# Performance work log

Measured on AMD Instinct MI355X. Metric: run time of the kernel, lower is better.

## Reference

```python
import jax, jax.numpy as jnp
import numpy as np

RNN_DIM = 256
HN_DIM = 2 * RNN_DIM            # bidirectional
EMB = 300                       # WORD_VEC_DIM
VD = 256                        # visual_dim
NHEAD = 2
DH = VD // NHEAD
N, SEQ, VH, VW = 16, 20, 32, 32
EPS = 1e-5


def layernorm(x, g, b):
    m = jnp.mean(x, axis=-1, keepdims=True)
    v = jnp.var(x, axis=-1, keepdims=True)
    return (x - m) * jax.lax.rsqrt(v + EPS) * g + b


def generate_spatial(n, vh, vw):
    # standard 8-dim spatial coordinate features (text_objseg style)
    w = np.arange(vw, dtype=np.float32)
    h = np.arange(vh, dtype=np.float32)
    xmin = w / vw * 2 - 1; xmax = (w + 1) / vw * 2 - 1
    ymin = h / vh * 2 - 1; ymax = (h + 1) / vh * 2 - 1
    f = np.zeros((vh, vw, 8), np.float32)
    f[..., 0] = xmin[None, :]; f[..., 1] = ymin[:, None]
    f[..., 2] = xmax[None, :]; f[..., 3] = ymax[:, None]
    f[..., 4] = (xmin + xmax)[None, :] / 2; f[..., 5] = (ymin + ymax)[:, None] / 2
    f[..., 6] = 1.0 / vw; f[..., 7] = 1.0 / vh
    return np.broadcast_to(f, (n, vh, vw, 8))  # NHWC


def setup_inputs():
    key = jax.random.key(0)
    ks = jax.random.split(key, 12)
    s = 0.02
    return {
        "hs": jax.random.normal(ks[0], (N, SEQ, HN_DIM), jnp.float32),
        "hn": jax.random.normal(ks[1], (N, HN_DIM), jnp.float32),
        "feature": jax.random.normal(ks[2], (N, VD, VH, VW), jnp.float32),
        "embedding": jax.random.normal(ks[3], (N, SEQ, EMB), jnp.float32),
        "words": jax.random.randint(ks[4], (N, SEQ), 0, 100, jnp.int32),
        "qconv_w": jax.random.normal(ks[5], (VD, EMB), jnp.float32) * s,
        "qconv_b": jnp.zeros((VD,), jnp.float32),
        "mconv_w": jax.random.normal(ks[6], (VD, VD + 8 + HN_DIM, 3, 3), jnp.float32) * s,
        "mnorm_g": jnp.ones((VD,), jnp.float32), "mnorm_b": jnp.zeros((VD,), jnp.float32),
        "in_proj_w": jax.random.normal(ks[7], (3 * VD, VD), jnp.float32) * s,
        "in_proj_b": jnp.zeros((3 * VD,), jnp.float32),
        "out_proj_w": jax.random.normal(ks[8], (VD, VD), jnp.float32) * s,
        "out_proj_b": jnp.zeros((VD,), jnp.float32),
        "norm_g": jnp.ones((VD,), jnp.float32), "norm_b": jnp.zeros((VD,), jnp.float32),
        "lin1_w": jax.random.normal(ks[9], (VD, VD), jnp.float32) * s,
        "lin1_b": jnp.zeros((VD,), jnp.float32),
        "lin2_w": jax.random.normal(ks[10], (VD, VD), jnp.float32) * s,
        "lin2_b": jnp.zeros((VD,), jnp.float32),
        "normf_g": jnp.ones((VD,), jnp.float32), "normf_b": jnp.zeros((VD,), jnp.float32),
    }


def _forward(hs, hn, feature, embedding, words,
             qconv_w, qconv_b, mconv_w, mnorm_g, mnorm_b,
             in_proj_w, in_proj_b, out_proj_w, out_proj_b,
             norm_g, norm_b, lin1_w, lin1_b, lin2_w, lin2_b, normf_g, normf_b):
    Nn, C, vh, vw = feature.shape
    P = vh * vw
    spatial = jnp.asarray(generate_spatial(Nn, vh, vw)).transpose(0, 3, 1, 2)  # (N,8,vh,vw)
    hn_rep = jnp.broadcast_to(hn[:, :, None, None], (Nn, hn.shape[1], vh, vw))
    Wq, Wk, Wv = jnp.split(in_proj_w, 3, axis=0)
    bq, bk, bv = jnp.split(in_proj_b, 3, axis=0)
    scale = 1.0 / np.sqrt(DH)

    def step(feat, xs):
        emb_n, active = xs  # emb_n: (N,EMB), active: bool scalar (words[0,n] != 0)
        q = jax.nn.relu(emb_n @ qconv_w.T + qconv_b)            # (N,VD)
        Q = jnp.broadcast_to(q[:, None, :], (Nn, P, VD))
        t = jnp.concatenate([feat, spatial, hn_rep], axis=1)    # (N,VD+8+HN,vh,vw)
        t = jax.lax.conv_general_dilated(t, mconv_w, (1, 1), "SAME",
                                         dimension_numbers=("NCHW", "OIHW", "NCHW"))
        t = jax.nn.relu(t).transpose(0, 2, 3, 1).reshape(Nn, P, VD)
        t = layernorm(t, mnorm_g, mnorm_b)                      # V = K = t
        # torch nn.MultiheadAttention default batch_first=False:
        # axis0 (=N) is the sequence axis, axis1 (=P) is the batch axis.
        qh = (Q @ Wq.T + bq).reshape(Nn, P, NHEAD, DH)
        kh = (t @ Wk.T + bk).reshape(Nn, P, NHEAD, DH)
        vv = (t @ Wv.T + bv).reshape(Nn, P, NHEAD, DH)
        attn = jax.nn.softmax(jnp.einsum("lphd,mphd->phlm", qh, kh) * scale, axis=-1)
        o = jnp.einsum("phlm,mphd->lphd", attn, vv).reshape(Nn, P, VD)
        fea = layernorm(t + (o @ out_proj_w.T + out_proj_b), norm_g, norm_b)
        f2 = jax.nn.relu(fea @ lin1_w.T + lin1_b) @ lin2_w.T + lin2_b
        fea = layernorm(fea + f2, normf_g, normf_b)
        new_feat = fea.transpose(0, 2, 1).reshape(Nn, VD, vh, vw)
        return jnp.where(active, new_feat, feat), None

    xs = (embedding.transpose(1, 0, 2), words[0, :] != 0)
    feat, _ = jax.lax.scan(step, feature, xs)
    return feat


def reference(hs, hn, feature, embedding, words,
              qconv_w, qconv_b, mconv_w, mnorm_g, mnorm_b,
              in_proj_w, in_proj_b, out_proj_w, out_proj_b,
              norm_g, norm_b, lin1_w, lin1_b, lin2_w, lin2_b, normf_g, normf_b):
    return _forward(hs, hn, feature, embedding, words,
                    qconv_w, qconv_b, mconv_w, mnorm_g, mnorm_b,
                    in_proj_w, in_proj_b, out_proj_w, out_proj_b,
                    norm_g, norm_b, lin1_w, lin1_b, lin2_w, lin2_b, normf_g, normf_b)
```

## Files before the change

### kernel.cpp

```cpp
#include <hip/hip_runtime.h>
#include <hip/hip_bf16.h>
#include <cstddef>

typedef __hip_bfloat16 bf16;
typedef short short8 __attribute__((ext_vector_type(8)));
typedef short short4v __attribute__((ext_vector_type(4)));
typedef float float4v __attribute__((ext_vector_type(4)));
#define DEV static __device__ __forceinline__

constexpr int NB = 16;
constexpr int SEQL = 20;
constexpr int CD = 256;
constexpr int PP = 1024;
constexpr int HND = 512;
constexpr int EMBD = 300;
constexpr int CIN = 776;

constexpr size_t SZB = (size_t)NB * PP * CD / 2;
constexpr size_t OF_FEATB = 0;
constexpr size_t OF_TB   = 1*SZB;
constexpr size_t OF_KHB  = 2*SZB;
constexpr size_t OF_VVB  = 3*SZB;
constexpr size_t OF_QH   = 7*SZB;
constexpr size_t OF_HNW  = OF_QH  + (size_t)SEQL*NB*CD;
constexpr size_t OF_SCV  = OF_HNW + (size_t)9*NB*CD;
constexpr size_t OF_WRG  = OF_SCV + (size_t)PP*CD;
constexpr size_t OF_AW   = OF_WRG + (size_t)9*CD*HND;
constexpr size_t OF_PK   = OF_AW  + (size_t)294912;
constexpr size_t OF_FLAG = OF_PK  + (size_t)163840;

DEV float bf2f(bf16 v) { return __bfloat162float(v); }
DEV bf16 f2bf(float v) { return __float2bfloat16(v); }
DEV float sh2f(short v) { bf16 t; *(short*)&t = v; return __bfloat162float(t); }
DEV short f2sh(float v) { bf16 t = f2bf(v); return *(const short*)&t; }

DEV float LD(const void* p, size_t i, int bf) {
  return bf ? __bfloat162float(((const bf16*)p)[i]) : ((const float*)p)[i];
}
DEV int get_bf(const float* ws) { return ((const int*)ws)[OF_FLAG]; }

__global__ void k_detect(const void* g, float* ws) {
  if (threadIdx.x == 0 && blockIdx.x == 0) {
    unsigned w = *(const unsigned*)g;
    ((int*)ws)[OF_FLAG] = ((w & 0xFFFFu) != 0u) ? 1 : 0;
  }
}

DEV void ln_reduce512(const float* tile, float* red, int tid) {
  const int x = tid & 31, seg = tid >> 5;
  float s = 0.f, sq = 0.f;
#pragma unroll
  for (int i = 0; i < 16; ++i) {
    float v = tile[(seg*16 + i)*33 + x];
    s += v; sq += v*v;
  }
  red[seg*32 + x] = s;
  red[512 + seg*32 + x] = sq;
  __syncthreads();
  if (tid < 32) {
    float ts = 0.f, tq = 0.f;
#pragma unroll
    for (int g = 0; g < 16; ++g) { ts += red[g*32 + tid]; tq += red[512 + g*32 + tid]; }
    float m = ts * (1.f/CD);
    float var = tq * (1.f/CD) - m*m;
    red[1024 + tid] = m;
    red[1056 + tid] = 1.f / sqrtf(var + 1e-5f);
  }
  __syncthreads();
}

DEV void mfma_core512(const short* __restrict__ As, const short* __restrict__ PKg,
                      int w, int lane, float4v acc[2][2]) {
  const int xb = lane & 15, quad = lane >> 4;
  const short* base = PKg + lane*8;
  short8 b0[8], b1[8];
#pragma unroll
  for (int ch = 0; ch < 8; ++ch) {
    b0[ch] = *(const short8*)&base[(size_t)((w*2+0)*8 + ch)*512];
    b1[ch] = *(const short8*)&base[(size_t)((w*2+1)*8 + ch)*512];
  }
#pragma unroll
  for (int ch = 0; ch < 8; ++ch) {
    short8 a0 = *(const short8*)&As[xb*264 + ch*32 + quad*8];
    short8 a1 = *(const short8*)&As[(16+xb)*264 + ch*32 + quad*8];
    acc[0][0] = __builtin_amdgcn_mfma_f32_16x16x32_bf16(a0, b0[ch], acc[0][0], 0, 0, 0);
    acc[0][1] = __builtin_amdgcn_mfma_f32_16x16x32_bf16(a0, b1[ch], acc[0][1], 0, 0, 0);
    acc[1][0] = __builtin_amdgcn_mfma_f32_16x16x32_bf16(a1, b0[ch], acc[1][0], 0, 0, 0);
    acc[1][1] = __builtin_amdgcn_mfma_f32_16x16x32_bf16(a1, b1[ch], acc[1][1], 0, 0, 0);
  }
}


__global__ __launch_bounds__(256) void k_init(const void* __restrict__ f, float* __restrict__ ws) {
  const int bf = get_bf(ws);
  const int b = blockIdx.x;
  const int n = b >> 10, p = b & 1023;
  const int c = threadIdx.x;
  bf16* fb = (bf16*)(ws + OF_FEATB);
  fb[(size_t)b*CD + c] = f2bf(LD(f, ((size_t)n*CD + c)*PP + p, bf));
}

__global__ __launch_bounds__(256) void k_qh(const void* __restrict__ emb, const void* __restrict__ qw,
                                            const void* __restrict__ qb, const void* __restrict__ ipw,
                                            const void* __restrict__ ipb, float* __restrict__ ws) {
  const int bf = get_bf(ws);
  const int b = blockIdx.x, s = b / NB, n = b % NB;
  const int o = threadIdx.x;
  __shared__ float se[EMBD];
  __shared__ float sq[CD];
  for (int i = o; i < EMBD; i += CD) se[i] = LD(emb, ((size_t)n*SEQL + s)*EMBD + i, bf);
  __syncthreads();
  float a = LD(qb, o, bf);
  if (bf) {
    const bf16* wr = (const bf16*)qw + (size_t)o*EMBD;
    for (int c = 0; c < EMBD; ++c) a += se[c]*bf2f(wr[c]);
  } else {
    const float* wr = (const float*)qw + (size_t)o*EMBD;
    for (int c = 0; c < EMBD; ++c) a += se[c]*wr[c];
  }
  sq[o] = fmaxf(a, 0.f);
  __syncthreads();
  float a2 = LD(ipb, o, bf);
  if (bf) {
    const bf16* wq = (const bf16*)ipw + (size_t)o*CD;
    for (int c = 0; c < CD; ++c) a2 += sq[c]*bf2f(wq[c]);
  } else {
    const float* wq = (const float*)ipw + (size_t)o*CD;
    for (int c = 0; c < CD; ++c) a2 += sq[c]*wq[c];
  }
  ws[OF_QH + ((size_t)s*NB + n)*CD + o] = a2;
}

__global__ __launch_bounds__(256) void k_wregion(const void* __restrict__ mw, float* __restrict__ ws) {
  const int bf = get_bf(ws);
  const int gid = blockIdx.x*256 + threadIdx.x;
  const int c = gid & (HND-1);
  const int o = (gid >> 9) & (CD-1);
  const int r = gid >> 17;
  const int ry = r/3, rx = r%3;
  float s = 0.f;
  for (int dy = 0; dy < 3; ++dy) {
    if (ry == 0 && dy == 0) continue;
    if (ry == 2 && dy == 2) continue;
    for (int dx = 0; dx < 3; ++dx) {
      if (rx == 0 && dx == 0) continue;
      if (rx == 2 && dx == 2) continue;
      s += LD(mw, ((size_t)o*CIN + 264 + c)*9 + dy*3 + dx, bf);
    }
  }
  ws[OF_WRG + gid] = s;
}

__global__ __launch_bounds__(256) void k_hnw(const void* __restrict__ hn, float* __restrict__ ws) {
  const int bf = get_bf(ws);
  const int b = blockIdx.x, r = b / NB, n = b % NB;
  const int o = threadIdx.x;
  __shared__ float sh[HND];
  for (int i = o; i < HND; i += CD) sh[i] = LD(hn, (size_t)n*HND + i, bf);
  __syncthreads();
  const float* wr = ws + OF_WRG + ((size_t)r*CD + o)*HND;
  float a = 0.f;
  for (int c = 0; c < HND; ++c) a += sh[c]*wr[c];
  ws[OF_HNW + ((size_t)r*NB + n)*CD + o] = a;
}

DEV float spat(int c, int yy, int xx) {
  switch (c) {
    case 0: return xx*(1.f/16) - 1.f;
    case 1: return yy*(1.f/16) - 1.f;
    case 2: return (xx+1)*(1.f/16) - 1.f;
    case 3: return (yy+1)*(1.f/16) - 1.f;
    case 4: return (xx+0.5f)*(1.f/16) - 1.f;
    case 5: return (yy+0.5f)*(1.f/16) - 1.f;
    default: return 1.f/32;
  }
}

__global__ __launch_bounds__(256) void k_sconv(const void* __restrict__ mw, float* __restrict__ ws) {
  const int bf = get_bf(ws);
  const int p = blockIdx.x, o = threadIdx.x;
  const int y = p >> 5, x = p & 31;
  float a = 0.f;
  for (int c = 0; c < 8; ++c)
    for (int dy = 0; dy < 3; ++dy) {
      int yy = y + dy - 1; if ((unsigned)yy >= 32u) continue;
      for (int dx = 0; dx < 3; ++dx) {
        int xx = x + dx - 1; if ((unsigned)xx >= 32u) continue;
        a += LD(mw, ((size_t)o*CIN + 256 + c)*9 + dy*3 + dx, bf) * spat(c, yy, xx);
      }
    }
  ws[OF_SCV + (size_t)p*CD + o] = a;
}

__global__ __launch_bounds__(256) void k_wpack(const void* __restrict__ mw, float* __restrict__ ws) {
  const int bf = get_bf(ws);
  const int idx = blockIdx.x*256 + threadIdx.x;
  const int j = idx & 7;
  const int lane = (idx >> 3) & 63;
  const int mt = (idx >> 9) & 15;
  const int ch = (idx >> 13) & 7;
  const int tap = idx >> 16;
  const int o = mt*16 + (lane & 15);
  const int c = ch*32 + (lane >> 4)*8 + j;
  bf16* aw = (bf16*)(ws + OF_AW);
  aw[idx] = f2bf(LD(mw, ((size_t)o*CIN + c)*9 + tap, bf));
}

__global__ __launch_bounds__(256) void k_wpackB(const void* __restrict__ ipw, const void* __restrict__ opw,
                                                const void* __restrict__ l1w, const void* __restrict__ l2w,
                                                float* __restrict__ ws) {
  const int bf = get_bf(ws);
  const int idx = blockIdx.x*256 + threadIdx.x;
  const int j = idx & 7;
  const int lane = (idx >> 3) & 63;
  const int ch = (idx >> 9) & 7;
  const int nt = (idx >> 12) & 15;
  const int g = idx >> 16;
  const int o = nt*16 + (lane & 15);
  const int k = ch*32 + (lane >> 4)*8 + j;
  float v;
  switch (g) {
    case 0: v = LD(ipw, ((size_t)(256 + o))*CD + k, bf); break;
    case 1: v = LD(ipw, ((size_t)(512 + o))*CD + k, bf); break;
    case 2: v = LD(opw, (size_t)o*CD + k, bf);           break;
    case 3: v = LD(l1w, (size_t)o*CD + k, bf);           break;
    default: v = LD(l2w, (size_t)o*CD + k, bf);          break;
  }
  ((bf16*)(ws + OF_PK))[idx] = f2bf(v);
}


__global__ __launch_bounds__(512, 4) void k_convkv(const void* __restrict__ mg, const void* __restrict__ mbv,
                                                   const void* __restrict__ ipb, float* __restrict__ ws) {
  __shared__ float smem[13464];
  short* Xs = (short*)smem;
  float* red  = smem;
  short* AsT  = (short*)(smem + 576);
  const int bfv = get_bf(ws);
  const int b = blockIdx.x, n = b >> 5, y = b & 31;
  const int tid = threadIdx.x;
  const int w = tid >> 6, lane = tid & 63;
  const int xb = lane & 15, quad = lane >> 4;
  const bf16* fb = (const bf16*)(ws + OF_FEATB);

  const short8 zero8 = {0,0,0,0,0,0,0,0};
  if (tid < 192) {
    const int r = tid >> 6, xp = ((tid >> 5) & 1) * 33, c0 = (tid & 31)*8;
    *(short8*)&Xs[(r*34 + xp)*264 + c0] = zero8;
  }
#pragma unroll
  for (int u = 0; u < 6; ++u) {
    const int lin = u*512 + tid;
    const int cgrp = lin & 31, xl = (lin >> 5) & 31, r = lin >> 10;
    const int row = y + r - 1;
    short8 v = zero8;
    if ((unsigned)row < 32u)
      v = *(const short8*)&fb[((size_t)(n*PP + row*32 + xl))*CD + cgrp*8];
    *(short8*)&Xs[(r*34 + 1 + xl)*264 + cgrp*8] = v;
  }
  __syncthreads();

  float4v a00 = (float4v)0.f, a01 = (float4v)0.f, a10 = (float4v)0.f, a11 = (float4v)0.f;
  const bf16* AW = (const bf16*)(ws + OF_AW);
  const int bvec = xb*264 + quad*8;

  short8 A0[3], A1[3], B0[3], B1[3];
#define PF(GI, S) do {                                                        \
    const int tap_ = (GI) >> 3, ch_ = (GI) & 7;                               \
    const int dy_ = (tap_ >= 6) ? 2 : ((tap_ >= 3) ? 1 : 0);                  \
    const int dx_ = tap_ - 3*dy_;                                             \
    const bf16* ap_ = AW + (((size_t)(tap_*8 + ch_)*16 + w*2)*64 + lane)*8;   \
    A0[S] = *(const short8*)&ap_[0];                                          \
    A1[S] = *(const short8*)&ap_[512];                                        \
    const short* bp_ = &Xs[(dy_*34 + dx_)*264 + ch_*32 + bvec];               \
    B0[S] = *(const short8*)&bp_[0];                                          \
    B1[S] = *(const short8*)&bp_[16*264];                                     \
  } while (0)

  PF(0, 0); PF(1, 1); PF(2, 2);
#pragma unroll
  for (int gi = 0; gi < 72; ++gi) {
    const int s = gi % 3;
    a00 = __builtin_amdgcn_mfma_f32_16x16x32_bf16(A0[s], B0[s], a00, 0, 0, 0);
    a01 = __builtin_amdgcn_mfma_f32_16x16x32_bf16(A0[s], B1[s], a01, 0, 0, 0);
    a10 = __builtin_amdgcn_mfma_f32_16x16x32_bf16(A1[s], B0[s], a10, 0, 0, 0);
    a11 = __builtin_amdgcn_mfma_f32_16x16x32_bf16(A1[s], B1[s], a11, 0, 0, 0);
    if (gi < 69) PF(gi + 3, s);
  }
#undef PF
  __syncthreads();

  const int o0 = w*32 + quad*4;
  const int o1 = o0 + 16;
  const int x0 = xb, x1 = 16 + xb;
  float v00[4], v01[4], v10[4], v11[4];
  {
    const int ry = (y == 0) ? 0 : ((y == 31) ? 2 : 1);
    const float* hnw = ws + OF_HNW;
    float4 hL0 = *(const float4*)&hnw[((size_t)(ry*3+0)*NB + n)*CD + o0];
    float4 hM0 = *(const float4*)&hnw[((size_t)(ry*3+1)*NB + n)*CD + o0];
    float4 hR0 = *(const float4*)&hnw[((size_t)(ry*3+2)*NB + n)*CD + o0];
    float4 hL1 = *(const float4*)&hnw[((size_t)(ry*3+0)*NB + n)*CD + o1];
    float4 hM1 = *(const float4*)&hnw[((size_t)(ry*3+1)*NB + n)*CD + o1];
    float4 hR1 = *(const float4*)&hnw[((size_t)(ry*3+2)*NB + n)*CD + o1];
    const float* scv = ws + OF_SCV + (size_t)(y*32)*CD;
    float4 s00 = *(const float4*)&scv[(size_t)x0*CD + o0];
    float4 s10 = *(const float4*)&scv[(size_t)x0*CD + o1];
    float4 s01 = *(const float4*)&scv[(size_t)x1*CD + o0];
    float4 s11 = *(const float4*)&scv[(size_t)x1*CD + o1];
    float4 h00 = (x0 == 0)  ? hL0 : hM0;
    float4 h10 = (x0 == 0)  ? hL1 : hM1;
    float4 h01 = (x1 == 31) ? hR0 : hM0;
    float4 h11 = (x1 == 31) ? hR1 : hM1;
    const float* s00p = (const float*)&s00; const float* s10p = (const float*)&s10;
    const float* s01p = (const float*)&s01; const float* s11p = (const float*)&s11;
    const float* h00p = (const float*)&h00; const float* h10p = (const float*)&h10;
    const float* h01p = (const float*)&h01; const float* h11p = (const float*)&h11;
#pragma unroll
    for (int r = 0; r < 4; ++r) {
      v00[r] = fmaxf(a00[r] + s00p[r] + h00p[r], 0.f);
      v10[r] = fmaxf(a10[r] + s10p[r] + h10p[r], 0.f);
      v01[r] = fmaxf(a01[r] + s01p[r] + h01p[r], 0.f);
      v11[r] = fmaxf(a11[r] + s11p[r] + h11p[r], 0.f);
    }
  }
  float sum0 = 0.f, sq0 = 0.f, sum1 = 0.f, sq1 = 0.f;
#pragma unroll
  for (int r = 0; r < 4; ++r) {
    sum0 += v00[r] + v10[r]; sq0 += v00[r]*v00[r] + v10[r]*v10[r];
    sum1 += v01[r] + v11[r]; sq1 += v01[r]*v01[r] + v11[r]*v11[r];
  }
  sum0 += __shfl_xor(sum0, 16, 64); sum0 += __shfl_xor(sum0, 32, 64);
  sq0  += __shfl_xor(sq0, 16, 64);  sq0  += __shfl_xor(sq0, 32, 64);
  sum1 += __shfl_xor(sum1, 16, 64); sum1 += __shfl_xor(sum1, 32, 64);
  sq1  += __shfl_xor(sq1, 16, 64);  sq1  += __shfl_xor(sq1, 32, 64);
  if (quad == 0) {
    red[x0*8 + w] = sum0;  red[256 + x0*8 + w] = sq0;
    red[x1*8 + w] = sum1;  red[256 + x1*8 + w] = sq1;
  }
  __syncthreads();
  if (tid < 32) {
    float ts = 0.f, tq = 0.f;
#pragma unroll
    for (int g = 0; g < 8; ++g) { ts += red[tid*8 + g]; tq += red[256 + tid*8 + g]; }
    float m = ts * (1.f/CD);
    float var = tq * (1.f/CD) - m*m;
    red[512 + tid] = m;
    red[544 + tid] = 1.f / sqrtf(var + 1e-5f);
  }
  __syncthreads();
  {
    const float m0 = red[512 + x0], r0 = red[544 + x0];
    const float m1 = red[512 + x1], r1 = red[544 + x1];
    float g0[4], b0[4], g1[4], b1[4];
#pragma unroll
    for (int r = 0; r < 4; ++r) {
      g0[r] = LD(mg, o0 + r, bfv); b0[r] = LD(mbv, o0 + r, bfv);
      g1[r] = LD(mg, o1 + r, bfv); b1[r] = LD(mbv, o1 + r, bfv);
    }
    short4v t00, t10, t01, t11;
#pragma unroll
    for (int r = 0; r < 4; ++r) {
      t00[r] = f2sh((v00[r] - m0)*r0*g0[r] + b0[r]);
      t10[r] = f2sh((v10[r] - m0)*r0*g1[r] + b1[r]);
      t01[r] = f2sh((v01[r] - m1)*r1*g0[r] + b0[r]);
      t11[r] = f2sh((v11[r] - m1)*r1*g1[r] + b1[r]);
    }
    *(short4v*)&AsT[x0*264 + o0] = t00;
    *(short4v*)&AsT[x0*264 + o1] = t10;
    *(short4v*)&AsT[x1*264 + o0] = t01;
    *(short4v*)&AsT[x1*264 + o1] = t11;
  }
  __syncthreads();

  {
    bf16* tp = (bf16*)(ws + OF_TB) + ((size_t)n*PP + (size_t)y*32)*CD;
    const int r = tid >> 4, c0 = (tid & 15)*16;
#pragma unroll
    for (int i = 0; i < 2; ++i) {
      short8 v = *(const short8*)&AsT[r*264 + c0 + i*8];
      *(short8*)&tp[(size_t)r*CD + c0 + i*8] = v;
    }
  }

  const short* PK = (const short*)(ws + OF_PK);
  const int p0 = y << 5;
#pragma unroll 1
  for (int G = 0; G < 2; ++G) {
    float4v ac2[2][2];
#pragma unroll
    for (int mt = 0; mt < 2; ++mt) { ac2[mt][0] = (float4v)0.f; ac2[mt][1] = (float4v)0.f; }
    mfma_core512(AsT, PK + (size_t)G*65536, w, lane, ac2);
    bf16* dst = (bf16*)(ws + (G ? OF_VVB : OF_KHB)) + ((size_t)n*PP + p0)*CD;
#pragma unroll
    for (int i = 0; i < 2; ++i) {
      const int c = (w*2 + i)*16 + xb;
      const float bias = LD(ipb, (size_t)(G+1)*256 + c, bfv);
#pragma unroll
      for (int mt = 0; mt < 2; ++mt)
#pragma unroll
        for (int r = 0; r < 4; ++r)
          dst[(size_t)(mt*16 + quad*4 + r)*CD + c] = f2bf(ac2[mt][i][r] + bias);
    }
  }
}

__global__ __launch_bounds__(512, 4) void k_oplin(const void* __restrict__ opb, const void* __restrict__ ng,
                                                  const void* __restrict__ nbv, const void* __restrict__ l1b,
                                                  const void* __restrict__ l2b, const void* __restrict__ nfg,
                                                  const void* __restrict__ nfb, const int* __restrict__ words,
                                                  int s, float* __restrict__ ws) {
  __shared__ float smem[15040];
  float* tile = smem;
  float* red  = smem + 8448;
  short* AsT  = (short*)smem;
  short* AsF  = (short*)(smem + 9536);
  short* SQb  = (short*)smem;
  short* SKs  = (short*)(smem + 4224);
  short* SVs  = (short*)(smem + 9536);
  short* Pb   = (short*)(smem + 13760);
  const int bf = get_bf(ws);
  const int b = blockIdx.x, p0 = b*2;
  const int tid = threadIdx.x, w = tid >> 6, lane = tid & 63;
  const int xb = lane & 15, quad = lane >> 4;
  const int o = tid & 255, half = tid >> 8;
  const short* PK = (const short*)(ws + OF_PK);
  const int c0i = (w*2 + 0)*16 + xb;
  const int c1i = (w*2 + 1)*16 + xb;

  {
    const int l = tid >> 5, c0 = (tid & 31)*8;
    const float* src = ws + OF_QH + ((size_t)(s*NB + l))*CD + c0;
    float4 q0 = *(const float4*)&src[0];
    float4 q1 = *(const float4*)&src[4];
    short8 t;
    t[0] = f2sh(q0.x); t[1] = f2sh(q0.y); t[2] = f2sh(q0.z); t[3] = f2sh(q0.w);
    t[4] = f2sh(q1.x); t[5] = f2sh(q1.y); t[6] = f2sh(q1.z); t[7] = f2sh(q1.w);
    *(short8*)&SQb[l*264 + c0] = t;
  }
  {
    const int row = tid >> 4, c0 = (tid & 15)*16;
    const int pp = row >> 4, l = row & 15;
    const size_t srcoff = ((size_t)l*PP + (p0 + pp))*CD + c0;
    const bf16* khb = (const bf16*)(ws + OF_KHB);
    const bf16* vvb = (const bf16*)(ws + OF_VVB);
    *(short8*)&SKs[row*264 + c0]     = *(const short8*)&khb[srcoff];
    *(short8*)&SKs[row*264 + c0 + 8] = *(const short8*)&khb[srcoff + 8];
    *(short8*)&SVs[row*264 + c0]     = *(const short8*)&vvb[srcoff];
    *(short8*)&SVs[row*264 + c0 + 8] = *(const short8*)&vvb[srcoff + 8];
  }
  __syncthreads();

  if (w < 4) {
    const int aq = w >> 1, hq = w & 1;
    float4v sacc = (float4v)0.f;
#pragma unroll
    for (int ch = 0; ch < 4; ++ch) {
      short8 qa = *(const short8*)&SQb[xb*264 + hq*128 + ch*32 + quad*8];
      short8 kb = *(const short8*)&SKs[(aq*16 + xb)*264 + hq*128 + ch*32 + quad*8];
      sacc = __builtin_amdgcn_mfma_f32_16x16x32_bf16(qa, kb, sacc, 0, 0, 0);
    }
#pragma unroll
    for (int r = 0; r < 4; ++r) {
      float sc = sacc[r] * 0.08838834764831845f;
      float mx = sc;
      mx = fmaxf(mx, __shfl_xor(mx, 1, 64));
      mx = fmaxf(mx, __shfl_xor(mx, 2, 64));
      mx = fmaxf(mx, __shfl_xor(mx, 4, 64));
      mx = fmaxf(mx, __shfl_xor(mx, 8, 64));
      float e = __expf(sc - mx);
      float su = e;
      su += __shfl_xor(su, 1, 64);
      su += __shfl_xor(su, 2, 64);
      su += __shfl_xor(su, 4, 64);
      su += __shfl_xor(su, 8, 64);
      Pb[(w*16 + quad*4 + r)*18 + xb] = f2sh(e / su);
    }
  }
  __syncthreads();

  {
    const int u = w >> 1, ap = u >> 1, hp = u & 1, dh = w & 1;
    short8 pa = {0,0,0,0,0,0,0,0};
    if (quad < 2) pa = *(const short8*)&Pb[(u*16 + xb)*18 + quad*8];
#pragma unroll
    for (int t = 0; t < 4; ++t) {
      const int dcol = hp*128 + dh*64 + t*16 + xb;
      short8 vb;
#pragma unroll
      for (int j = 0; j < 8; ++j)
        vb[j] = SVs[(ap*16 + (quad & 1)*8 + j)*264 + dcol];
      float4v acc = (float4v)0.f;
      acc = __builtin_amdgcn_mfma_f32_16x16x32_bf16(pa, vb, acc, 0, 0, 0);
#pragma unroll
      for (int r = 0; r < 4; ++r)
        AsT[(ap*16 + quad*4 + r)*264 + dcol] = f2sh(acc[r]);
    }
  }
  __syncthreads();

  float vo[2][2][4];
  {
    float4v acc[2][2];
#pragma unroll
    for (int mt = 0; mt < 2; ++mt) { acc[mt][0] = (float4v)0.f; acc[mt][1] = (float4v)0.f; }
    mfma_core512(AsT, PK + (size_t)2*65536, w, lane, acc);
    const float bo0 = LD(opb, c0i, bf), bo1 = LD(opb, c1i, bf);
    const bf16* tb = (const bf16*)(ws + OF_TB);
#pragma unroll
    for (int mt = 0; mt < 2; ++mt)
#pragma unroll
      for (int r = 0; r < 4; ++r) {
        const int x = mt*16 + quad*4 + r;
        const size_t prow = ((size_t)(x & 15)*PP + p0 + (x >> 4))*CD;
        vo[mt][0][r] = acc[mt][0][r] + bo0 + bf2f(tb[prow + c0i]);
        vo[mt][1][r] = acc[mt][1][r] + bo1 + bf2f(tb[prow + c1i]);
      }
  }
  __syncthreads();
#pragma unroll
  for (int i = 0; i < 2; ++i)
#pragma unroll
    for (int mt = 0; mt < 2; ++mt)
#pragma unroll
      for (int r = 0; r < 4; ++r)
        tile[((w*2 + i)*16 + xb)*33 + mt*16 + quad*4 + r] = vo[mt][i][r];
  __syncthreads();
  ln_reduce512(tile, red, tid);
  {
    const float g = LD(ng, o, bf), bb = LD(nbv, o, bf);
#pragma unroll
    for (int xi = 0; xi < 16; ++xi) {
      const int x = half*16 + xi;
      AsF[x*264 + o] = f2sh((tile[o*33 + x] - red[1024 + x]) * red[1056 + x] * g + bb);
    }
  }
  __syncthreads();

  {
    float4v acc[2][2];
#pragma unroll
    for (int mt = 0; mt < 2; ++mt) { acc[mt][0] = (float4v)0.f; acc[mt][1] = (float4v)0.f; }
    mfma_core512(AsF, PK + (size_t)3*65536, w, lane, acc);
#pragma unroll
    for (int i = 0; i < 2; ++i) {
      const int c = (w*2 + i)*16 + xb;
      const float bias = LD(l1b, c, bf);
#pragma unroll
      for (int mt = 0; mt < 2; ++mt)
#pragma unroll
        for (int r = 0; r < 4; ++r)
          AsT[(mt*16 + quad*4 + r)*264 + c] = f2sh(fmaxf(acc[mt][i][r] + bias, 0.f));
    }
  }
  __syncthreads();

  {
    float4v acc[2][2];
#pragma unroll
    for (int mt = 0; mt < 2; ++mt) { acc[mt][0] = (float4v)0.f; acc[mt][1] = (float4v)0.f; }
    mfma_core512(AsT, PK + (size_t)4*65536, w, lane, acc);
    const float bl0 = LD(l2b, c0i, bf), bl1 = LD(l2b, c1i, bf);
#pragma unroll
    for (int mt = 0; mt < 2; ++mt)
#pragma unroll
      for (int r = 0; r < 4; ++r) {
        const int x = mt*16 + quad*4 + r;
        vo[mt][0][r] = acc[mt][0][r] + bl0 + sh2f(AsF[x*264 + c0i]);
        vo[mt][1][r] = acc[mt][1][r] + bl1 + sh2f(AsF[x*264 + c1i]);
      }
  }
  __syncthreads();
#pragma unroll
  for (int i = 0; i < 2; ++i)
#pragma unroll
    for (int mt = 0; mt < 2; ++mt)
#pragma unroll
      for (int r = 0; r < 4; ++r)
        tile[((w*2 + i)*16 + xb)*33 + mt*16 + quad*4 + r] = vo[mt][i][r];
  __syncthreads();
  ln_reduce512(tile, red, tid);
  if (words[s] != 0) {
    const float g = LD(nfg, o, bf), b2 = LD(nfb, o, bf);
    bf16* fbd = (bf16*)(ws + OF_FEATB);
#pragma unroll
    for (int xi = 0; xi < 16; ++xi) {
      const int x = half*16 + xi;
      fbd[((size_t)(x & 15)*PP + p0 + (x >> 4))*CD + o] =
          f2bf((tile[o*33 + x] - red[1024 + x]) * red[1056 + x] * g + b2);
    }
  }
}

__global__ __launch_bounds__(256) void k_final(const float* __restrict__ ws, void* __restrict__ out) {
  const int bf = get_bf(ws);
  const size_t i = (size_t)blockIdx.x*256 + threadIdx.x;
  const int n = (int)(i >> 18), c = (int)((i >> 10) & 255), p = (int)(i & 1023);
  const bf16* fb = (const bf16*)(ws + OF_FEATB);
  float v = bf2f(fb[((size_t)(n*PP + p))*CD + c]);
  if (bf) ((bf16*)out)[i] = f2bf(v);
  else    ((float*)out)[i] = v;
}

extern "C" void kernel_launch(void* const* d_in, const int* in_sizes, int n_in,
                              void* d_out, int out_size, void* d_ws, size_t ws_size,
                              hipStream_t stream) {
  (void)in_sizes; (void)n_in; (void)out_size; (void)ws_size;
  const void* hn      = d_in[1];
  const void* feature = d_in[2];
  const void* emb     = d_in[3];
  const int*  words   = (const int*)d_in[4];
  const void* qw  = d_in[5];
  const void* qb  = d_in[6];
  const void* mw  = d_in[7];
  const void* mg  = d_in[8];
  const void* mb  = d_in[9];
  const void* ipw = d_in[10];
  const void* ipb = d_in[11];
  const void* opw = d_in[12];
  const void* opb = d_in[13];
  const void* ng  = d_in[14];
  const void* nb  = d_in[15];
  const void* l1w = d_in[16];
  const void* l1b = d_in[17];
  const void* l2w = d_in[18];
  const void* l2b = d_in[19];
  const void* nfg = d_in[20];
  const void* nfb = d_in[21];
  float* ws = (float*)d_ws;

  k_detect<<<1, 64, 0, stream>>>(mg, ws);
  k_init<<<NB*PP, 256, 0, stream>>>(feature, ws);
  k_qh<<<SEQL*NB, 256, 0, stream>>>(emb, qw, qb, ipw, ipb, ws);
  k_wregion<<<(9*CD*HND)/256, 256, 0, stream>>>(mw, ws);
  k_hnw<<<9*NB, 256, 0, stream>>>(hn, ws);
  k_sconv<<<PP, 256, 0, stream>>>(mw, ws);
  k_wpack<<<(9*8*16*64*8)/256, 256, 0, stream>>>(mw, ws);
  k_wpackB<<<(5*65536)/256, 256, 0, stream>>>(ipw, opw, l1w, l2w, ws);

  for (int s = 0; s < SEQL; ++s) {
    k_convkv<<<NB*32, 512, 0, stream>>>(mg, mb, ipb, ws);
    k_oplin<<<PP/2, 512, 0, stream>>>(opb, ng, nb, l1b, l2b, nfg, nfb, words, s, ws);
  }
  k_final<<<NB*CD*PP/256, 256, 0, stream>>>(ws, (void*)d_out);
}
```

Baseline: 1.383 ms.

## Process two image rows per conv block with 1024 threads, each wave owning 16 channels

The conv+KV kernel now handles two output rows per block using 16 waves instead of one row with 8 waves. Each wave owns 16 output channels and reuses one weight fragment across both rows, so weight loads per output are halved and the 3-row halo overhead becomes 4 rows per 2 outputs. The K/V projection also keeps its B fragments in registers and reuses them across both row groups. In exchange the grid has half as many blocks (256), there is more shared memory and register pressure, and occupancy may drop.

```diff
diff --git a/kernel.cpp b/kernel.cpp
--- a/kernel.cpp
+++ b/kernel.cpp
@@ -230,29 +230,30 @@
 }
 
 
-__global__ __launch_bounds__(512, 4) void k_convkv(const void* __restrict__ mg, const void* __restrict__ mbv,
-                                                   const void* __restrict__ ipb, float* __restrict__ ws) {
-  __shared__ float smem[13464];
+__global__ __launch_bounds__(1024, 4) void k_convkv(const void* __restrict__ mg, const void* __restrict__ mbv,
+                                                    const void* __restrict__ ipb, float* __restrict__ ws) {
+  __shared__ float smem[17952];
   short* Xs = (short*)smem;
   float* red  = smem;
-  short* AsT  = (short*)(smem + 576);
+  short* AsT  = (short*)(smem + 2176);
   const int bfv = get_bf(ws);
-  const int b = blockIdx.x, n = b >> 5, y = b & 31;
+  const int b = blockIdx.x, n = b >> 4, yp = b & 15;
+  const int y0 = yp*2;
   const int tid = threadIdx.x;
   const int w = tid >> 6, lane = tid & 63;
   const int xb = lane & 15, quad = lane >> 4;
   const bf16* fb = (const bf16*)(ws + OF_FEATB);
 
   const short8 zero8 = {0,0,0,0,0,0,0,0};
-  if (tid < 192) {
+  if (tid < 256) {
     const int r = tid >> 6, xp = ((tid >> 5) & 1) * 33, c0 = (tid & 31)*8;
     *(short8*)&Xs[(r*34 + xp)*264 + c0] = zero8;
   }
 #pragma unroll
-  for (int u = 0; u < 6; ++u) {
-    const int lin = u*512 + tid;
+  for (int u = 0; u < 4; ++u) {
+    const int lin = u*1024 + tid;
     const int cgrp = lin & 31, xl = (lin >> 5) & 31, r = lin >> 10;
-    const int row = y + r - 1;
+    const int row = y0 + r - 1;
     short8 v = zero8;
     if ((unsigned)row < 32u)
       v = *(const short8*)&fb[((size_t)(n*PP + row*32 + xl))*CD + cgrp*8];
@@ -260,121 +261,106 @@
   }
   __syncthreads();
 
-  float4v a00 = (float4v)0.f, a01 = (float4v)0.f, a10 = (float4v)0.f, a11 = (float4v)0.f;
+  float4v acc[2][2];
+#pragma unroll
+  for (int rr = 0; rr < 2; ++rr) { acc[rr][0] = (float4v)0.f; acc[rr][1] = (float4v)0.f; }
   const bf16* AW = (const bf16*)(ws + OF_AW);
   const int bvec = xb*264 + quad*8;
 
-  short8 A0[3], A1[3], B0[3], B1[3];
+  short8 A0[3], B00[3], B01[3], B10[3], B11[3];
 #define PF(GI, S) do {                                                        \
     const int tap_ = (GI) >> 3, ch_ = (GI) & 7;                               \
     const int dy_ = (tap_ >= 6) ? 2 : ((tap_ >= 3) ? 1 : 0);                  \
     const int dx_ = tap_ - 3*dy_;                                             \
-    const bf16* ap_ = AW + (((size_t)(tap_*8 + ch_)*16 + w*2)*64 + lane)*8;   \
+    const bf16* ap_ = AW + (((size_t)(tap_*8 + ch_)*16 + w)*64 + lane)*8;     \
     A0[S] = *(const short8*)&ap_[0];                                          \
-    A1[S] = *(const short8*)&ap_[512];                                        \
-    const short* bp_ = &Xs[(dy_*34 + dx_)*264 + ch_*32 + bvec];               \
-    B0[S] = *(const short8*)&bp_[0];                                          \
-    B1[S] = *(const short8*)&bp_[16*264];                                     \
+    const short* bp0_ = &Xs[(dy_*34 + dx_)*264 + ch_*32 + bvec];              \
+    B00[S] = *(const short8*)&bp0_[0];                                        \
+    B01[S] = *(const short8*)&bp0_[16*264];                                   \
+    const short* bp1_ = bp0_ + 34*264;                                        \
+    B10[S] = *(const short8*)&bp1_[0];                                        \
+    B11[S] = *(const short8*)&bp1_[16*264];                                   \
   } while (0)
 
   PF(0, 0); PF(1, 1); PF(2, 2);
 #pragma unroll
   for (int gi = 0; gi < 72; ++gi) {
     const int s = gi % 3;
-    a00 = __builtin_amdgcn_mfma_f32_16x16x32_bf16(A0[s], B0[s], a00, 0, 0, 0);
-    a01 = __builtin_amdgcn_mfma_f32_16x16x32_bf16(A0[s], B1[s], a01, 0, 0, 0);
-    a10 = __builtin_amdgcn_mfma_f32_16x16x32_bf16(A1[s], B0[s], a10, 0, 0, 0);
-    a11 = __builtin_amdgcn_mfma_f32_16x16x32_bf16(A1[s], B1[s], a11, 0, 0, 0);
+    acc[0][0] = __builtin_amdgcn_mfma_f32_16x16x32_bf16(A0[s], B00[s], acc[0][0], 0, 0, 0);
+    acc[0][1] = __builtin_amdgcn_mfma_f32_16x16x32_bf16(A0[s], B01[s], acc[0][1], 0, 0, 0);
+    acc[1][0] = __builtin_amdgcn_mfma_f32_16x16x32_bf16(A0[s], B10[s], acc[1][0], 0, 0, 0);
+    acc[1][1] = __builtin_amdgcn_mfma_f32_16x16x32_bf16(A0[s], B11[s], acc[1][1], 0, 0, 0);
     if (gi < 69) PF(gi + 3, s);
   }
 #undef PF
   __syncthreads();
 
-  const int o0 = w*32 + quad*4;
-  const int o1 = o0 + 16;
-  const int x0 = xb, x1 = 16 + xb;
-  float v00[4], v01[4], v10[4], v11[4];
-  {
-    const int ry = (y == 0) ? 0 : ((y == 31) ? 2 : 1);
+  const int ob = w*16 + quad*4;
+  float vv[2][2][4];
+  float g4[4], b4[4];
+#pragma unroll
+  for (int r = 0; r < 4; ++r) { g4[r] = LD(mg, ob + r, bfv); b4[r] = LD(mbv, ob + r, bfv); }
+#pragma unroll
+  for (int rr = 0; rr < 2; ++rr) {
+    const int yr = y0 + rr;
+    const int ry = (yr == 0) ? 0 : ((yr == 31) ? 2 : 1);
     const float* hnw = ws + OF_HNW;
-    float4 hL0 = *(const float4*)&hnw[((size_t)(ry*3+0)*NB + n)*CD + o0];
-    float4 hM0 = *(const float4*)&hnw[((size_t)(ry*3+1)*NB + n)*CD + o0];
-    float4 hR0 = *(const float4*)&hnw[((size_t)(ry*3+2)*NB + n)*CD + o0];
-    float4 hL1 = *(const float4*)&hnw[((size_t)(ry*3+0)*NB + n)*CD + o1];
-    float4 hM1 = *(const float4*)&hnw[((size_t)(ry*3+1)*NB + n)*CD + o1];
-    float4 hR1 = *(const float4*)&hnw[((size_t)(ry*3+2)*NB + n)*CD + o1];
-    const float* scv = ws + OF_SCV + (size_t)(y*32)*CD;
-    float4 s00 = *(const float4*)&scv[(size_t)x0*CD + o0];
-    float4 s10 = *(const float4*)&scv[(size_t)x0*CD + o1];
-    float4 s01 = *(const float4*)&scv[(size_t)x1*CD + o0];
-    float4 s11 = *(const float4*)&scv[(size_t)x1*CD + o1];
-    float4 h00 = (x0 == 0)  ? hL0 : hM0;
-    float4 h10 = (x0 == 0)  ? hL1 : hM1;
-    float4 h01 = (x1 == 31) ? hR0 : hM0;
-    float4 h11 = (x1 == 31) ? hR1 : hM1;
-    const float* s00p = (const float*)&s00; const float* s10p = (const float*)&s10;
-    const float* s01p = (const float*)&s01; const float* s11p = (const float*)&s11;
-    const float* h00p = (const float*)&h00; const float* h10p = (const float*)&h10;
-    const float* h01p = (const float*)&h01; const float* h11p = (const float*)&h11;
-#pragma unroll
-    for (int r = 0; r < 4; ++r) {
-      v00[r] = fmaxf(a00[r] + s00p[r] + h00p[r], 0.f);
-      v10[r] = fmaxf(a10[r] + s10p[r] + h10p[r], 0.f);
-      v01[r] = fmaxf(a01[r] + s01p[r] + h01p[r], 0.f);
-      v11[r] = fmaxf(a11[r] + s11p[r] + h11p[r], 0.f);
-    }
-  }
-  float sum0 = 0.f, sq0 = 0.f, sum1 = 0.f, sq1 = 0.f;
-#pragma unroll
-  for (int r = 0; r < 4; ++r) {
-    sum0 += v00[r] + v10[r]; sq0 += v00[r]*v00[r] + v10[r]*v10[r];
-    sum1 += v01[r] + v11[r]; sq1 += v01[r]*v01[r] + v11[r]*v11[r];
-  }
-  sum0 += __shfl_xor(sum0, 16, 64); sum0 += __shfl_xor(sum0, 32, 64);
-  sq0  += __shfl_xor(sq0, 16, 64);  sq0  += __shfl_xor(sq0, 32, 64);
-  sum1 += __shfl_xor(sum1, 16, 64); sum1 += __shfl_xor(sum1, 32, 64);
-  sq1  += __shfl_xor(sq1, 16, 64);  sq1  += __shfl_xor(sq1, 32, 64);
-  if (quad == 0) {
-    red[x0*8 + w] = sum0;  red[256 + x0*8 + w] = sq0;
-    red[x1*8 + w] = sum1;  red[256 + x1*8 + w] = sq1;
-  }
-  __syncthreads();
-  if (tid < 32) {
+    float4 hL = *(const float4*)&hnw[((size_t)(ry*3+0)*NB + n)*CD + ob];
+    float4 hM = *(const float4*)&hnw[((size_t)(ry*3+1)*NB + n)*CD + ob];
+    float4 hR = *(const float4*)&hnw[((size_t)(ry*3+2)*NB + n)*CD + ob];
+    const float* scv = ws + OF_SCV + (size_t)(yr*32)*CD;
+#pragma unroll
+    for (int xh = 0; xh < 2; ++xh) {
+      const int x = xh*16 + xb;
+      float4 sc = *(const float4*)&scv[(size_t)x*CD + ob];
+      float4 hh = (x == 0) ? hL : ((x == 31) ? hR : hM);
+      const float* scp = (const float*)&sc;
+      const float* hhp = (const float*)&hh;
+#pragma unroll
+      for (int r = 0; r < 4; ++r)
+        vv[rr][xh][r] = fmaxf(acc[rr][xh][r] + scp[r] + hhp[r], 0.f);
+    }
+  }
+#pragma unroll
+  for (int rr = 0; rr < 2; ++rr)
+#pragma unroll
+    for (int xh = 0; xh < 2; ++xh) {
+      float s = 0.f, q = 0.f;
+#pragma unroll
+      for (int r = 0; r < 4; ++r) { s += vv[rr][xh][r]; q += vv[rr][xh][r]*vv[rr][xh][r]; }
+      s += __shfl_xor(s, 16, 64); s += __shfl_xor(s, 32, 64);
+      q += __shfl_xor(q, 16, 64); q += __shfl_xor(q, 32, 64);
+      if (quad == 0) {
+        red[(rr*32 + xh*16 + xb)*16 + w] = s;
+        red[1024 + (rr*32 + xh*16 + xb)*16 + w] = q;
+      }
+    }
+  __syncthreads();
+  if (tid < 64) {
     float ts = 0.f, tq = 0.f;
 #pragma unroll
-    for (int g = 0; g < 8; ++g) { ts += red[tid*8 + g]; tq += red[256 + tid*8 + g]; }
+    for (int g = 0; g < 16; ++g) { ts += red[tid*16 + g]; tq += red[1024 + tid*16 + g]; }
     float m = ts * (1.f/CD);
     float var = tq * (1.f/CD) - m*m;
-    red[512 + tid] = m;
-    red[544 + tid] = 1.f / sqrtf(var + 1e-5f);
-  }
-  __syncthreads();
-  {
-    const float m0 = red[512 + x0], r0 = red[544 + x0];
-    const float m1 = red[512 + x1], r1 = red[544 + x1];
-    float g0[4], b0[4], g1[4], b1[4];
-#pragma unroll
-    for (int r = 0; r < 4; ++r) {
-      g0[r] = LD(mg, o0 + r, bfv); b0[r] = LD(mbv, o0 + r, bfv);
-      g1[r] = LD(mg, o1 + r, bfv); b1[r] = LD(mbv, o1 + r, bfv);
-    }
-    short4v t00, t10, t01, t11;
-#pragma unroll
-    for (int r = 0; r < 4; ++r) {
-      t00[r] = f2sh((v00[r] - m0)*r0*g0[r] + b0[r]);
-      t10[r] = f2sh((v10[r] - m0)*r0*g1[r] + b1[r]);
-      t01[r] = f2sh((v01[r] - m1)*r1*g0[r] + b0[r]);
-      t11[r] = f2sh((v11[r] - m1)*r1*g1[r] + b1[r]);
-    }
-    *(short4v*)&AsT[x0*264 + o0] = t00;
-    *(short4v*)&AsT[x0*264 + o1] = t10;
-    *(short4v*)&AsT[x1*264 + o0] = t01;
-    *(short4v*)&AsT[x1*264 + o1] = t11;
-  }
-  __syncthreads();
-
-  {
-    bf16* tp = (bf16*)(ws + OF_TB) + ((size_t)n*PP + (size_t)y*32)*CD;
+    red[2048 + tid] = m;
+    red[2112 + tid] = 1.f / sqrtf(var + 1e-5f);
+  }
+  __syncthreads();
+#pragma unroll
+  for (int rr = 0; rr < 2; ++rr)
+#pragma unroll
+    for (int xh = 0; xh < 2; ++xh) {
+      const int px = rr*32 + xh*16 + xb;
+      const float m = red[2048 + px], rs = red[2112 + px];
+      short4v t;
+#pragma unroll
+      for (int r = 0; r < 4; ++r) t[r] = f2sh((vv[rr][xh][r] - m)*rs*g4[r] + b4[r]);
+      *(short4v*)&AsT[px*264 + ob] = t;
+    }
+  __syncthreads();
+
+  {
+    bf16* tp = (bf16*)(ws + OF_TB) + ((size_t)n*PP + (size_t)y0*32)*CD;
     const int r = tid >> 4, c0 = (tid & 15)*16;
 #pragma unroll
     for (int i = 0; i < 2; ++i) {
@@ -384,23 +370,34 @@
   }
 
   const short* PK = (const short*)(ws + OF_PK);
-  const int p0 = y << 5;
+  const int p0 = y0 << 5;
 #pragma unroll 1
   for (int G = 0; G < 2; ++G) {
-    float4v ac2[2][2];
-#pragma unroll
-    for (int mt = 0; mt < 2; ++mt) { ac2[mt][0] = (float4v)0.f; ac2[mt][1] = (float4v)0.f; }
-    mfma_core512(AsT, PK + (size_t)G*65536, w, lane, ac2);
+    const short* PKg = PK + (size_t)G*65536;
+    const short* base = PKg + lane*8;
+    short8 bfr[8];
+#pragma unroll
+    for (int ch = 0; ch < 8; ++ch)
+      bfr[ch] = *(const short8*)&base[(size_t)(w*8 + ch)*512];
     bf16* dst = (bf16*)(ws + (G ? OF_VVB : OF_KHB)) + ((size_t)n*PP + p0)*CD;
-#pragma unroll
-    for (int i = 0; i < 2; ++i) {
-      const int c = (w*2 + i)*16 + xb;
-      const float bias = LD(ipb, (size_t)(G+1)*256 + c, bfv);
+    const int c = w*16 + xb;
+    const float bias = LD(ipb, (size_t)(G+1)*256 + c, bfv);
+#pragma unroll 1
+    for (int rg = 0; rg < 2; ++rg) {
+      float4v ac2[2];
+      ac2[0] = (float4v)0.f; ac2[1] = (float4v)0.f;
+#pragma unroll
+      for (int ch = 0; ch < 8; ++ch) {
+        short8 a0 = *(const short8*)&AsT[(rg*32 + xb)*264 + ch*32 + quad*8];
+        short8 a1 = *(const short8*)&AsT[(rg*32 + 16 + xb)*264 + ch*32 + quad*8];
+        ac2[0] = __builtin_amdgcn_mfma_f32_16x16x32_bf16(a0, bfr[ch], ac2[0], 0, 0, 0);
+        ac2[1] = __builtin_amdgcn_mfma_f32_16x16x32_bf16(a1, bfr[ch], ac2[1], 0, 0, 0);
+      }
 #pragma unroll
       for (int mt = 0; mt < 2; ++mt)
 #pragma unroll
         for (int r = 0; r < 4; ++r)
-          dst[(size_t)(mt*16 + quad*4 + r)*CD + c] = f2bf(ac2[mt][i][r] + bias);
+          dst[(size_t)(rg*32 + mt*16 + quad*4 + r)*CD + c] = f2bf(ac2[mt][r] + bias);
     }
   }
 }
@@ -639,7 +636,7 @@
   k_wpackB<<<(5*65536)/256, 256, 0, stream>>>(ipw, opw, l1w, l2w, ws);
 
   for (int s = 0; s < SEQL; ++s) {
-    k_convkv<<<NB*32, 512, 0, stream>>>(mg, mb, ipb, ws);
+    k_convkv<<<NB*16, 1024, 0, stream>>>(mg, mb, ipb, ws);
     k_oplin<<<PP/2, 512, 0, stream>>>(opb, ng, nb, l1b, l2b, nfg, nfb, words, s, ws);
   }
   k_final<<<NB*CD*PP/256, 256, 0, stream>>>(ws, (void*)d_out);
```

Result: slower. 2.222 ms (+60.7%).

## Fuse K/V projection into attention kernel to avoid global K/V round-trip

Applied to the files above, without the earlier changes.

The K and V in-projection GEMMs move out of the conv kernel and into the attention/out-proj kernel. There each block loads its tile of t into shared memory once, computes K and V directly into LDS, and reuses the same tile for the residual add. This removes the per-step global write and read of two full bf16 K/V tensors. In exchange, shared memory per block grows, and the projection GEMMs now run in the second kernel, which may change occupancy and load balance.

```diff
diff --git a/kernel.cpp b/kernel.cpp
--- a/kernel.cpp
+++ b/kernel.cpp
@@ -19,8 +19,6 @@
 constexpr size_t SZB = (size_t)NB * PP * CD / 2;
 constexpr size_t OF_FEATB = 0;
 constexpr size_t OF_TB   = 1*SZB;
-constexpr size_t OF_KHB  = 2*SZB;
-constexpr size_t OF_VVB  = 3*SZB;
 constexpr size_t OF_QH   = 7*SZB;
 constexpr size_t OF_HNW  = OF_QH  + (size_t)SEQL*NB*CD;
 constexpr size_t OF_SCV  = OF_HNW + (size_t)9*NB*CD;
@@ -242,6 +240,7 @@
   const int w = tid >> 6, lane = tid & 63;
   const int xb = lane & 15, quad = lane >> 4;
   const bf16* fb = (const bf16*)(ws + OF_FEATB);
+  (void)ipb;
 
   const short8 zero8 = {0,0,0,0,0,0,0,0};
   if (tid < 192) {
@@ -382,35 +381,14 @@
       *(short8*)&tp[(size_t)r*CD + c0 + i*8] = v;
     }
   }
-
-  const short* PK = (const short*)(ws + OF_PK);
-  const int p0 = y << 5;
-#pragma unroll 1
-  for (int G = 0; G < 2; ++G) {
-    float4v ac2[2][2];
-#pragma unroll
-    for (int mt = 0; mt < 2; ++mt) { ac2[mt][0] = (float4v)0.f; ac2[mt][1] = (float4v)0.f; }
-    mfma_core512(AsT, PK + (size_t)G*65536, w, lane, ac2);
-    bf16* dst = (bf16*)(ws + (G ? OF_VVB : OF_KHB)) + ((size_t)n*PP + p0)*CD;
-#pragma unroll
-    for (int i = 0; i < 2; ++i) {
-      const int c = (w*2 + i)*16 + xb;
-      const float bias = LD(ipb, (size_t)(G+1)*256 + c, bfv);
-#pragma unroll
-      for (int mt = 0; mt < 2; ++mt)
-#pragma unroll
-        for (int r = 0; r < 4; ++r)
-          dst[(size_t)(mt*16 + quad*4 + r)*CD + c] = f2bf(ac2[mt][i][r] + bias);
-    }
-  }
-}
-
-__global__ __launch_bounds__(512, 4) void k_oplin(const void* __restrict__ opb, const void* __restrict__ ng,
-                                                  const void* __restrict__ nbv, const void* __restrict__ l1b,
-                                                  const void* __restrict__ l2b, const void* __restrict__ nfg,
-                                                  const void* __restrict__ nfb, const int* __restrict__ words,
-                                                  int s, float* __restrict__ ws) {
-  __shared__ float smem[15040];
+}
+
+__global__ __launch_bounds__(512, 4) void k_oplin(const void* __restrict__ ipb, const void* __restrict__ opb,
+                                                  const void* __restrict__ ng, const void* __restrict__ nbv,
+                                                  const void* __restrict__ l1b, const void* __restrict__ l2b,
+                                                  const void* __restrict__ nfg, const void* __restrict__ nfb,
+                                                  const int* __restrict__ words, int s, float* __restrict__ ws) {
+  __shared__ float smem[18560];
   float* tile = smem;
   float* red  = smem + 8448;
   short* AsT  = (short*)smem;
@@ -419,6 +397,7 @@
   short* SKs  = (short*)(smem + 4224);
   short* SVs  = (short*)(smem + 9536);
   short* Pb   = (short*)(smem + 13760);
+  short* Tt   = (short*)(smem + 14336);
   const int bf = get_bf(ws);
   const int b = blockIdx.x, p0 = b*2;
   const int tid = threadIdx.x, w = tid >> 6, lane = tid & 63;
@@ -442,12 +421,29 @@
     const int row = tid >> 4, c0 = (tid & 15)*16;
     const int pp = row >> 4, l = row & 15;
     const size_t srcoff = ((size_t)l*PP + (p0 + pp))*CD + c0;
-    const bf16* khb = (const bf16*)(ws + OF_KHB);
-    const bf16* vvb = (const bf16*)(ws + OF_VVB);
-    *(short8*)&SKs[row*264 + c0]     = *(const short8*)&khb[srcoff];
-    *(short8*)&SKs[row*264 + c0 + 8] = *(const short8*)&khb[srcoff + 8];
-    *(short8*)&SVs[row*264 + c0]     = *(const short8*)&vvb[srcoff];
-    *(short8*)&SVs[row*264 + c0 + 8] = *(const short8*)&vvb[srcoff + 8];
+    const bf16* tb = (const bf16*)(ws + OF_TB);
+    *(short8*)&Tt[row*264 + c0]     = *(const short8*)&tb[srcoff];
+    *(short8*)&Tt[row*264 + c0 + 8] = *(const short8*)&tb[srcoff + 8];
+  }
+  __syncthreads();
+
+#pragma unroll 1
+  for (int G = 0; G < 2; ++G) {
+    float4v acc[2][2];
+#pragma unroll
+    for (int mt = 0; mt < 2; ++mt) { acc[mt][0] = (float4v)0.f; acc[mt][1] = (float4v)0.f; }
+    mfma_core512(Tt, PK + (size_t)G*65536, w, lane, acc);
+    short* dstS = G ? SVs : SKs;
+#pragma unroll
+    for (int i = 0; i < 2; ++i) {
+      const int c = (w*2 + i)*16 + xb;
+      const float bias = LD(ipb, (size_t)(G+1)*256 + c, bf);
+#pragma unroll
+      for (int mt = 0; mt < 2; ++mt)
+#pragma unroll
+        for (int r = 0; r < 4; ++r)
+          dstS[(mt*16 + quad*4 + r)*264 + c] = f2sh(acc[mt][i][r] + bias);
+    }
   }
   __syncthreads();
 
@@ -506,15 +502,13 @@
     for (int mt = 0; mt < 2; ++mt) { acc[mt][0] = (float4v)0.f; acc[mt][1] = (float4v)0.f; }
     mfma_core512(AsT, PK + (size_t)2*65536, w, lane, acc);
     const float bo0 = LD(opb, c0i, bf), bo1 = LD(opb, c1i, bf);
-    const bf16* tb = (const bf16*)(ws + OF_TB);
 #pragma unroll
     for (int mt = 0; mt < 2; ++mt)
 #pragma unroll
       for (int r = 0; r < 4; ++r) {
         const int x = mt*16 + quad*4 + r;
-        const size_t prow = ((size_t)(x & 15)*PP + p0 + (x >> 4))*CD;
-        vo[mt][0][r] = acc[mt][0][r] + bo0 + bf2f(tb[prow + c0i]);
-        vo[mt][1][r] = acc[mt][1][r] + bo1 + bf2f(tb[prow + c1i]);
+        vo[mt][0][r] = acc[mt][0][r] + bo0 + sh2f(Tt[x*264 + c0i]);
+        vo[mt][1][r] = acc[mt][1][r] + bo1 + sh2f(Tt[x*264 + c1i]);
       }
   }
   __syncthreads();
@@ -640,7 +634,7 @@
 
   for (int s = 0; s < SEQL; ++s) {
     k_convkv<<<NB*32, 512, 0, stream>>>(mg, mb, ipb, ws);
-    k_oplin<<<PP/2, 512, 0, stream>>>(opb, ng, nb, l1b, l2b, nfg, nfb, words, s, ws);
+    k_oplin<<<PP/2, 512, 0, stream>>>(ipb, opb, ng, nb, l1b, l2b, nfg, nfb, words, s, ws);
   }
   k_final<<<NB*CD*PP/256, 256, 0, stream>>>(ws, (void*)d_out);
 }
```

Result: no change. 1.372 ms (-0.8%).
